# Optimization experiments

Hardware: AMD Instinct MI355X
Metric: run time of the kernel (lower is better)

Reference implementation:

```python
import jax, jax.numpy as jnp
import numpy as np

D = 1024            # BIGNET_DIM
GS = 16             # group_size
NG = D * D // GS    # groups per layer = 65536
N_LAYERS = 18       # 6 blocks * 3 linears
LORA_LAYERS = {0: 0, 6: 1, 12: 2}  # linear index -> lora slot (first linear of blocks 0,2,4)
RANK = 32
BATCH = 16384
EPS = 1e-5


def setup_inputs() -> dict:
    key = jax.random.key(0)
    ks = jax.random.split(key, 6)
    x = jax.random.normal(ks[0], (BATCH, D), dtype=jnp.float32)
    w_q = jax.random.randint(ks[1], (N_LAYERS, NG, GS), 0, 16, dtype=jnp.int32)
    w_norm = jax.random.uniform(ks[2], (N_LAYERS, NG, 1), dtype=jnp.float32)
    bias = jax.random.normal(ks[3], (N_LAYERS, D), dtype=jnp.float32) * 0.02
    lora_a = jax.random.normal(ks[4], (3, RANK, D), dtype=jnp.float32) * (1.0 / np.sqrt(D))
    lora_b = jax.random.normal(ks[5], (3, D, RANK), dtype=jnp.float32) * 0.02
    ln_w = jnp.ones((6, D), dtype=jnp.float32)
    ln_b = jnp.zeros((6, D), dtype=jnp.float32)
    return {"x": x, "w_q": w_q, "w_norm": w_norm, "bias": bias,
            "lora_a": lora_a, "lora_b": lora_b, "ln_w": ln_w, "ln_b": ln_b}


def _dequant(q, n):
    # block_dequantize_4bit: codes in [0,15] -> [-norm, +norm] per group
    return ((q.astype(jnp.float32) / 15.0) * 2.0 - 1.0) * n  # [NG, GS]


def reference(x, w_q, w_norm, bias, lora_a, lora_b, ln_w, ln_b):
    h = x
    for blk in range(6):
        for pos in range(3):
            l = blk * 3 + pos
            W = _dequant(w_q[l], w_norm[l]).reshape(D, D)  # [out, in]
            out = h @ W.T + bias[l]
            if l in LORA_LAYERS:
                i = LORA_LAYERS[l]
                out = out + (h @ lora_a[i].T) @ lora_b[i].T
            if pos < 2:
                out = jax.nn.relu(out)
            h = out
        mu = jnp.mean(h, axis=-1, keepdims=True)
        var = jnp.mean(jnp.square(h - mu), axis=-1, keepdims=True)
        h = (h - mu) * jax.lax.rsqrt(var + EPS) * ln_w[blk] + ln_b[blk]
    return h
```

## Files before the change

### kernel.cpp

```cpp
#include <hip/hip_runtime.h>
#include <cstdint>
#include <cstddef>


typedef short  bf16x8 __attribute__((ext_vector_type(8)));
typedef float  f32x4  __attribute__((ext_vector_type(4)));

__device__ __forceinline__ unsigned short f2bf(float f) {
  unsigned int u = __builtin_bit_cast(unsigned int, f);
  u += 0x7FFFu + ((u >> 16) & 1u);
  return (unsigned short)(u >> 16);
}

__device__ __forceinline__ void async_copy16(void* lds, const void* g) {
  __builtin_amdgcn_global_load_lds(
      (const __attribute__((address_space(1))) void*)(uintptr_t)(g),
      (__attribute__((address_space(3))) void*)(unsigned int)(uintptr_t)(lds),
      16, 0, 0);
}

__global__ __launch_bounds__(256) void dequant_kernel(
    const int* __restrict__ wq, const float* __restrict__ wn,
    const float* __restrict__ lora_a, const float* __restrict__ lora_b,
    unsigned short* __restrict__ Wbf) {
  const int l   = blockIdx.y;
  const int t   = threadIdx.x;
  const int blk = blockIdx.x;
  const long base = (long)l * 1048576;
  const float s = 2.0f / 15.0f;

  int4  q[4];
  float nrm[4];
#pragma unroll
  for (int k = 0; k < 4; ++k) {
    const int i4 = blk * 1024 + k * 256 + t;
    q[k]   = *(const int4*)(wq + base + (long)i4 * 4);
    nrm[k] = wn[l * 65536 + (i4 >> 2)];
  }

  float v[4][4];
#pragma unroll
  for (int k = 0; k < 4; ++k) {
    v[k][0] = ((float)q[k].x * s - 1.0f) * nrm[k];
    v[k][1] = ((float)q[k].y * s - 1.0f) * nrm[k];
    v[k][2] = ((float)q[k].z * s - 1.0f) * nrm[k];
    v[k][3] = ((float)q[k].w * s - 1.0f) * nrm[k];
  }

  const int slot = (l == 0) ? 0 : (l == 6) ? 1 : (l == 12) ? 2 : -1;
  if (slot >= 0) {
    const float* A = lora_a + slot * 32768 + t * 4;
    const float* B = lora_b + slot * 32768 + blk * 128;
#pragma unroll 8
    for (int r = 0; r < 32; ++r) {
      const float4 a4 = *(const float4*)(A + r * 1024);
#pragma unroll
      for (int k = 0; k < 4; ++k) {
        const float br = B[k * 32 + r];
        v[k][0] = fmaf(br, a4.x, v[k][0]);
        v[k][1] = fmaf(br, a4.y, v[k][1]);
        v[k][2] = fmaf(br, a4.z, v[k][2]);
        v[k][3] = fmaf(br, a4.w, v[k][3]);
      }
    }
  }

#pragma unroll
  for (int k = 0; k < 4; ++k) {
    unsigned short u[4] = {f2bf(v[k][0]), f2bf(v[k][1]),
                           f2bf(v[k][2]), f2bf(v[k][3])};
    const long e0 = base + ((long)blk * 1024 + k * 256 + t) * 4;
    *(uint2*)(Wbf + e0) = *(uint2*)u;
  }
}

__global__ __launch_bounds__(256) void cvt_bf16_kernel(
    const float* __restrict__ in, unsigned short* __restrict__ out) {
  const long b0 = (long)blockIdx.x * 4096 + threadIdx.x * 4;
  float4 v[4];
#pragma unroll
  for (int k = 0; k < 4; ++k) v[k] = *(const float4*)(in + b0 + k * 1024);
#pragma unroll
  for (int k = 0; k < 4; ++k) {
    unsigned short u[4] = {f2bf(v[k].x), f2bf(v[k].y), f2bf(v[k].z), f2bf(v[k].w)};
    *(ushort4*)(out + b0 + k * 1024) = *(ushort4*)u;
  }
}

template <int MODE>
__global__ __launch_bounds__(256, 4) void gemm_kernel(
    const unsigned short* __restrict__ H,
    const unsigned short* __restrict__ W,
    const float* __restrict__ bias,
    unsigned short* __restrict__ outb,
    float* __restrict__ outf) {
  constexpr int K = 1024;
  constexpr int NN = 1024;

  __shared__ uint4 ldsq[2048];
  char* base = (char*)ldsq;

  const int tid = threadIdx.x;
  const int w   = tid >> 6;
  const int ln  = tid & 63;
  const int b   = blockIdx.x;
  const int m0  = ((b & 7) * 16 + (b >> 6)) * 128;
  const int n0  = ((b >> 3) & 7) * 128;

  const int gc = (ln & 7) ^ (ln >> 3);
  const unsigned short* gA = H + (size_t)(m0 + w * 32 + (ln >> 3)) * K + gc * 8;
  const unsigned short* gB = W + (size_t)(n0 + w * 32 + (ln >> 3)) * K + gc * 8;
  char* ldsA = base + w * 4096;
  char* ldsB = base + 16384 + w * 4096;

  const int quad = ln >> 4;
  const int lrow = ln & 15;
  const int sw   = lrow & 7;
  const int c0   = ((quad)     ^ sw) * 16;
  const int c1   = ((quad + 4) ^ sw) * 16;
  const int wm   = (w >> 1) * 64;
  const int wn   = (w & 1) * 64;
  const char* fragA = base + (wm + lrow) * 128;
  const char* fragB = base + 16384 + (wn + lrow) * 128;

  f32x4 acc[4][4];
#pragma unroll
  for (int i = 0; i < 4; ++i)
#pragma unroll
    for (int j = 0; j < 4; ++j) acc[i][j] = (f32x4){0.f, 0.f, 0.f, 0.f};

  for (int kt = 0; kt < 16; ++kt) {
    const unsigned short* pA = gA + kt * 64;
    const unsigned short* pB = gB + kt * 64;
#pragma unroll
    for (int i = 0; i < 4; ++i) {
      async_copy16(ldsA + i * 1024, pA + (size_t)i * 8 * K);
      async_copy16(ldsB + i * 1024, pB + (size_t)i * 8 * K);
    }
    __syncthreads();
#pragma unroll
    for (int kk = 0; kk < 2; ++kk) {
      const int co = kk ? c1 : c0;
      bf16x8 af[4], bg[4];
#pragma unroll
      for (int mt = 0; mt < 4; ++mt)
        af[mt] = *(const bf16x8*)(fragA + mt * 2048 + co);
#pragma unroll
      for (int nt = 0; nt < 4; ++nt)
        bg[nt] = *(const bf16x8*)(fragB + nt * 2048 + co);
#pragma unroll
      for (int mt = 0; mt < 4; ++mt)
#pragma unroll
        for (int nt = 0; nt < 4; ++nt)
          acc[mt][nt] = __builtin_amdgcn_mfma_f32_16x16x32_bf16(
              af[mt], bg[nt], acc[mt][nt], 0, 0, 0);
    }
    __syncthreads();
  }

#pragma unroll
  for (int nt = 0; nt < 4; ++nt) {
    const int n = n0 + wn + nt * 16 + lrow;
    const float bs = bias[n];
#pragma unroll
    for (int mt = 0; mt < 4; ++mt) {
      const int mb = m0 + wm + mt * 16 + quad * 4;
      f32x4 v = acc[mt][nt];
#pragma unroll
      for (int r = 0; r < 4; ++r) {
        float o = v[r] + bs;
        if (MODE == 0) o = fmaxf(o, 0.0f);
        if (MODE == 1) {
          outf[(size_t)(mb + r) * NN + n] = o;
        } else {
          outb[(size_t)(mb + r) * NN + n] = f2bf(o);
        }
      }
    }
  }
}

__global__ __launch_bounds__(256) void ln_kernel(
    const float* __restrict__ in, const float* __restrict__ lnw,
    const float* __restrict__ lnb, unsigned short* __restrict__ outb,
    float* __restrict__ outf, int wbf, int wf32) {
  const int wv = threadIdx.x >> 6;
  const int ln = threadIdx.x & 63;
  const int row = blockIdx.x * 4 + wv;
  const float* p = in + (size_t)row * 1024;

  float4 v[4];
  float s = 0.f, q = 0.f;
#pragma unroll
  for (int c = 0; c < 4; ++c) {
    v[c] = *(const float4*)(p + c * 256 + ln * 4);
    s += v[c].x + v[c].y + v[c].z + v[c].w;
    q += v[c].x * v[c].x + v[c].y * v[c].y + v[c].z * v[c].z + v[c].w * v[c].w;
  }
#pragma unroll
  for (int off = 32; off; off >>= 1) {
    s += __shfl_xor(s, off);
    q += __shfl_xor(q, off);
  }
  const float mu  = s * (1.0f / 1024.0f);
  const float var = q * (1.0f / 1024.0f) - mu * mu;
  const float rs  = rsqrtf(var + 1e-5f);

#pragma unroll
  for (int c = 0; c < 4; ++c) {
    const int col = c * 256 + ln * 4;
    const float4 w4 = *(const float4*)(lnw + col);
    const float4 b4 = *(const float4*)(lnb + col);
    const float y0 = (v[c].x - mu) * rs * w4.x + b4.x;
    const float y1 = (v[c].y - mu) * rs * w4.y + b4.y;
    const float y2 = (v[c].z - mu) * rs * w4.z + b4.z;
    const float y3 = (v[c].w - mu) * rs * w4.w + b4.w;
    if (wbf) {
      unsigned short u[4] = {f2bf(y0), f2bf(y1), f2bf(y2), f2bf(y3)};
      *(ushort4*)(outb + (size_t)row * 1024 + col) = *(ushort4*)u;
    }
    if (wf32) {
      float4 y = make_float4(y0, y1, y2, y3);
      *(float4*)(outf + (size_t)row * 1024 + col) = y;
    }
  }
}

__global__ __launch_bounds__(256) void ln_bf16_kernel(
    const unsigned short* __restrict__ in, const float* __restrict__ lnw,
    const float* __restrict__ lnb, unsigned short* __restrict__ outb) {
  const int wv = threadIdx.x >> 6;
  const int ln = threadIdx.x & 63;
  const int row = blockIdx.x * 4 + wv;
  const unsigned short* p = in + (size_t)row * 1024 + ln * 16;

  const uint4 r0 = *(const uint4*)(p);
  const uint4 r1 = *(const uint4*)(p + 8);
  const unsigned ru[8] = {r0.x, r0.y, r0.z, r0.w, r1.x, r1.y, r1.z, r1.w};

  float f[16];
#pragma unroll
  for (int i = 0; i < 8; ++i) {
    f[2 * i]     = __builtin_bit_cast(float, ru[i] << 16);
    f[2 * i + 1] = __builtin_bit_cast(float, ru[i] & 0xffff0000u);
  }

  float s = 0.f, q = 0.f;
#pragma unroll
  for (int i = 0; i < 16; ++i) { s += f[i]; q += f[i] * f[i]; }
#pragma unroll
  for (int off = 32; off; off >>= 1) {
    s += __shfl_xor(s, off);
    q += __shfl_xor(q, off);
  }
  const float mu  = s * (1.0f / 1024.0f);
  const float var = q * (1.0f / 1024.0f) - mu * mu;
  const float rs  = rsqrtf(var + 1e-5f);

  const float* wp = lnw + ln * 16;
  const float* bp = lnb + ln * 16;
  unsigned o[8];
#pragma unroll
  for (int i = 0; i < 8; ++i) {
    const float y0 = (f[2 * i]     - mu) * rs * wp[2 * i]     + bp[2 * i];
    const float y1 = (f[2 * i + 1] - mu) * rs * wp[2 * i + 1] + bp[2 * i + 1];
    o[i] = (unsigned)f2bf(y0) | ((unsigned)f2bf(y1) << 16);
  }
  unsigned short* dst = outb + (size_t)row * 1024 + ln * 16;
  *(uint4*)(dst)     = make_uint4(o[0], o[1], o[2], o[3]);
  *(uint4*)(dst + 8) = make_uint4(o[4], o[5], o[6], o[7]);
}

extern "C" void kernel_launch(void* const* d_in, const int* in_sizes, int n_in,
                              void* d_out, int out_size, void* d_ws, size_t ws_size,
                              hipStream_t stream) {
  const float* x    = (const float*)d_in[0];
  const int*   wq   = (const int*)d_in[1];
  const float* wn   = (const float*)d_in[2];
  const float* bias = (const float*)d_in[3];
  const float* la   = (const float*)d_in[4];
  const float* lb   = (const float*)d_in[5];
  const float* lnw  = (const float*)d_in[6];
  const float* lnb  = (const float*)d_in[7];
  float* out = (float*)d_out;

  char* ws = (char*)d_ws;
  unsigned short* Wbf = (unsigned short*)ws;
  unsigned short* hA  = (unsigned short*)(ws + 37748736);
  unsigned short* hB  = (unsigned short*)(ws + 37748736 + 33554432);

  dequant_kernel<<<dim3(256, 18), 256, 0, stream>>>(wq, wn, la, lb, Wbf);
  cvt_bf16_kernel<<<4096, 256, 0, stream>>>(x, hA);

  for (int blk = 0; blk < 6; ++blk) {
    const int l = blk * 3;
    gemm_kernel<0><<<1024, 256, 0, stream>>>(
        hA, Wbf + (size_t)l * 1048576, bias + l * 1024, hB, nullptr);
    gemm_kernel<0><<<1024, 256, 0, stream>>>(
        hB, Wbf + (size_t)(l + 1) * 1048576, bias + (l + 1) * 1024, hA, nullptr);
    if (blk < 5) {
      gemm_kernel<2><<<1024, 256, 0, stream>>>(
          hA, Wbf + (size_t)(l + 2) * 1048576, bias + (l + 2) * 1024, hB, nullptr);
      ln_bf16_kernel<<<4096, 256, 0, stream>>>(
          hB, lnw + blk * 1024, lnb + blk * 1024, hA);
    } else {
      gemm_kernel<1><<<1024, 256, 0, stream>>>(
          hA, Wbf + (size_t)(l + 2) * 1048576, bias + (l + 2) * 1024, nullptr, out);
      ln_kernel<<<4096, 256, 0, stream>>>(
          out, lnw + blk * 1024, lnb + blk * 1024, nullptr, out, 0, 1);
    }
  }
}
```

Before: 922.5 us.

## Swap MFMA operands for vectorized epilogue stores and precompute LoRA product

Adds a SWAP variant of the GEMM that exchanges the MFMA A/B operands. Each lane then holds four consecutive output columns, so the epilogue can write bias-added results as packed vector stores instead of scattered scalar stores. The variant is used only for even blocks, which looks like an A/B experiment. The LoRA B·A product is moved out of the dequant kernel into a separate kernel that writes a dense fp32 matrix into the hB scratch buffer, and dequant then simply adds it. This adds an extra kernel launch and roughly 12 MB of traffic in exchange for removing redundant FMA loops in the dequant kernel.

```diff
diff --git a/kernel.cpp b/kernel.cpp
--- a/kernel.cpp
+++ b/kernel.cpp
@@ -19,9 +19,44 @@
       16, 0, 0);
 }
 
+__global__ __launch_bounds__(256) void lora_kernel(
+    const float* __restrict__ lora_a,
+    const float* __restrict__ lora_b,
+    float* __restrict__ LA) {
+  const int slot = blockIdx.y;
+  const int o0   = blockIdx.x * 4;
+  const int t    = threadIdx.x;
+  const float* A = lora_a + slot * 32768 + t * 4;
+  const float* B = lora_b + slot * 32768 + o0 * 32;
+
+  float acc[4][4];
+#pragma unroll
+  for (int k = 0; k < 4; ++k)
+#pragma unroll
+    for (int j = 0; j < 4; ++j) acc[k][j] = 0.f;
+
+#pragma unroll 8
+  for (int r = 0; r < 32; ++r) {
+    const float4 a4 = *(const float4*)(A + r * 1024);
+#pragma unroll
+    for (int k = 0; k < 4; ++k) {
+      const float br = B[k * 32 + r];
+      acc[k][0] = fmaf(br, a4.x, acc[k][0]);
+      acc[k][1] = fmaf(br, a4.y, acc[k][1]);
+      acc[k][2] = fmaf(br, a4.z, acc[k][2]);
+      acc[k][3] = fmaf(br, a4.w, acc[k][3]);
+    }
+  }
+#pragma unroll
+  for (int k = 0; k < 4; ++k) {
+    float4 o = make_float4(acc[k][0], acc[k][1], acc[k][2], acc[k][3]);
+    *(float4*)(LA + (size_t)slot * 1048576 + (size_t)(o0 + k) * 1024 + t * 4) = o;
+  }
+}
+
 __global__ __launch_bounds__(256) void dequant_kernel(
     const int* __restrict__ wq, const float* __restrict__ wn,
-    const float* __restrict__ lora_a, const float* __restrict__ lora_b,
+    const float* __restrict__ LA,
     unsigned short* __restrict__ Wbf) {
   const int l   = blockIdx.y;
   const int t   = threadIdx.x;
@@ -29,13 +64,24 @@
   const long base = (long)l * 1048576;
   const float s = 2.0f / 15.0f;
 
+  const int slot = (l == 0) ? 0 : (l == 6) ? 1 : (l == 12) ? 2 : -1;
+
   int4  q[4];
   float nrm[4];
+  float4 c4[4];
 #pragma unroll
   for (int k = 0; k < 4; ++k) {
     const int i4 = blk * 1024 + k * 256 + t;
     q[k]   = *(const int4*)(wq + base + (long)i4 * 4);
     nrm[k] = wn[l * 65536 + (i4 >> 2)];
+  }
+  if (slot >= 0) {
+    const float* LAp = LA + (size_t)slot * 1048576;
+#pragma unroll
+    for (int k = 0; k < 4; ++k) {
+      const int i4 = blk * 1024 + k * 256 + t;
+      c4[k] = *(const float4*)(LAp + (size_t)i4 * 4);
+    }
   }
 
   float v[4][4];
@@ -46,22 +92,11 @@
     v[k][2] = ((float)q[k].z * s - 1.0f) * nrm[k];
     v[k][3] = ((float)q[k].w * s - 1.0f) * nrm[k];
   }
-
-  const int slot = (l == 0) ? 0 : (l == 6) ? 1 : (l == 12) ? 2 : -1;
   if (slot >= 0) {
-    const float* A = lora_a + slot * 32768 + t * 4;
-    const float* B = lora_b + slot * 32768 + blk * 128;
-#pragma unroll 8
-    for (int r = 0; r < 32; ++r) {
-      const float4 a4 = *(const float4*)(A + r * 1024);
-#pragma unroll
-      for (int k = 0; k < 4; ++k) {
-        const float br = B[k * 32 + r];
-        v[k][0] = fmaf(br, a4.x, v[k][0]);
-        v[k][1] = fmaf(br, a4.y, v[k][1]);
-        v[k][2] = fmaf(br, a4.z, v[k][2]);
-        v[k][3] = fmaf(br, a4.w, v[k][3]);
-      }
+#pragma unroll
+    for (int k = 0; k < 4; ++k) {
+      v[k][0] += c4[k].x; v[k][1] += c4[k].y;
+      v[k][2] += c4[k].z; v[k][3] += c4[k].w;
     }
   }
 
@@ -87,7 +122,7 @@
   }
 }
 
-template <int MODE>
+template <int MODE, int SWAP>
 __global__ __launch_bounds__(256, 4) void gemm_kernel(
     const unsigned short* __restrict__ H,
     const unsigned short* __restrict__ W,
@@ -151,29 +186,60 @@
 #pragma unroll
       for (int mt = 0; mt < 4; ++mt)
 #pragma unroll
-        for (int nt = 0; nt < 4; ++nt)
-          acc[mt][nt] = __builtin_amdgcn_mfma_f32_16x16x32_bf16(
-              af[mt], bg[nt], acc[mt][nt], 0, 0, 0);
+        for (int nt = 0; nt < 4; ++nt) {
+          if (SWAP) {
+            acc[mt][nt] = __builtin_amdgcn_mfma_f32_16x16x32_bf16(
+                bg[nt], af[mt], acc[mt][nt], 0, 0, 0);
+          } else {
+            acc[mt][nt] = __builtin_amdgcn_mfma_f32_16x16x32_bf16(
+                af[mt], bg[nt], acc[mt][nt], 0, 0, 0);
+          }
+        }
     }
     __syncthreads();
   }
 
-#pragma unroll
-  for (int nt = 0; nt < 4; ++nt) {
-    const int n = n0 + wn + nt * 16 + lrow;
-    const float bs = bias[n];
+  if (SWAP) {
 #pragma unroll
     for (int mt = 0; mt < 4; ++mt) {
-      const int mb = m0 + wm + mt * 16 + quad * 4;
-      f32x4 v = acc[mt][nt];
-#pragma unroll
-      for (int r = 0; r < 4; ++r) {
-        float o = v[r] + bs;
-        if (MODE == 0) o = fmaxf(o, 0.0f);
+      const size_t row = (size_t)(m0 + wm + mt * 16 + lrow);
+#pragma unroll
+      for (int nt = 0; nt < 4; ++nt) {
+        const int nb = n0 + wn + nt * 16 + quad * 4;
+        const float4 bs = *(const float4*)(bias + nb);
+        const f32x4 v = acc[mt][nt];
+        float o0 = v[0] + bs.x, o1 = v[1] + bs.y;
+        float o2 = v[2] + bs.z, o3 = v[3] + bs.w;
+        if (MODE == 0) {
+          o0 = fmaxf(o0, 0.0f); o1 = fmaxf(o1, 0.0f);
+          o2 = fmaxf(o2, 0.0f); o3 = fmaxf(o3, 0.0f);
+        }
         if (MODE == 1) {
-          outf[(size_t)(mb + r) * NN + n] = o;
+          *(float4*)(outf + row * NN + nb) = make_float4(o0, o1, o2, o3);
         } else {
-          outb[(size_t)(mb + r) * NN + n] = f2bf(o);
+          unsigned short u[4] = {f2bf(o0), f2bf(o1), f2bf(o2), f2bf(o3)};
+          *(uint2*)(outb + row * NN + nb) = *(uint2*)u;
+        }
+      }
+    }
+  } else {
+#pragma unroll
+    for (int nt = 0; nt < 4; ++nt) {
+      const int n = n0 + wn + nt * 16 + lrow;
+      const float bs = bias[n];
+#pragma unroll
+      for (int mt = 0; mt < 4; ++mt) {
+        const int mb = m0 + wm + mt * 16 + quad * 4;
+        f32x4 v = acc[mt][nt];
+#pragma unroll
+        for (int r = 0; r < 4; ++r) {
+          float o = v[r] + bs;
+          if (MODE == 0) o = fmaxf(o, 0.0f);
+          if (MODE == 1) {
+            outf[(size_t)(mb + r) * NN + n] = o;
+          } else {
+            outb[(size_t)(mb + r) * NN + n] = f2bf(o);
+          }
         }
       }
     }
@@ -288,23 +354,38 @@
   unsigned short* Wbf = (unsigned short*)ws;
   unsigned short* hA  = (unsigned short*)(ws + 37748736);
   unsigned short* hB  = (unsigned short*)(ws + 37748736 + 33554432);
-
-  dequant_kernel<<<dim3(256, 18), 256, 0, stream>>>(wq, wn, la, lb, Wbf);
+  float* LA = (float*)hB;
+
+  lora_kernel<<<dim3(256, 3), 256, 0, stream>>>(la, lb, LA);
+  dequant_kernel<<<dim3(256, 18), 256, 0, stream>>>(wq, wn, LA, Wbf);
   cvt_bf16_kernel<<<4096, 256, 0, stream>>>(x, hA);
 
   for (int blk = 0; blk < 6; ++blk) {
     const int l = blk * 3;
-    gemm_kernel<0><<<1024, 256, 0, stream>>>(
-        hA, Wbf + (size_t)l * 1048576, bias + l * 1024, hB, nullptr);
-    gemm_kernel<0><<<1024, 256, 0, stream>>>(
-        hB, Wbf + (size_t)(l + 1) * 1048576, bias + (l + 1) * 1024, hA, nullptr);
-    if (blk < 5) {
-      gemm_kernel<2><<<1024, 256, 0, stream>>>(
+    if ((blk & 1) == 0) {
+      gemm_kernel<0, 1><<<1024, 256, 0, stream>>>(
+          hA, Wbf + (size_t)l * 1048576, bias + l * 1024, hB, nullptr);
+      gemm_kernel<0, 1><<<1024, 256, 0, stream>>>(
+          hB, Wbf + (size_t)(l + 1) * 1048576, bias + (l + 1) * 1024, hA, nullptr);
+      gemm_kernel<2, 1><<<1024, 256, 0, stream>>>(
+          hA, Wbf + (size_t)(l + 2) * 1048576, bias + (l + 2) * 1024, hB, nullptr);
+      ln_bf16_kernel<<<4096, 256, 0, stream>>>(
+          hB, lnw + blk * 1024, lnb + blk * 1024, hA);
+    } else if (blk < 5) {
+      gemm_kernel<0, 0><<<1024, 256, 0, stream>>>(
+          hA, Wbf + (size_t)l * 1048576, bias + l * 1024, hB, nullptr);
+      gemm_kernel<0, 0><<<1024, 256, 0, stream>>>(
+          hB, Wbf + (size_t)(l + 1) * 1048576, bias + (l + 1) * 1024, hA, nullptr);
+      gemm_kernel<2, 0><<<1024, 256, 0, stream>>>(
           hA, Wbf + (size_t)(l + 2) * 1048576, bias + (l + 2) * 1024, hB, nullptr);
       ln_bf16_kernel<<<4096, 256, 0, stream>>>(
           hB, lnw + blk * 1024, lnb + blk * 1024, hA);
     } else {
-      gemm_kernel<1><<<1024, 256, 0, stream>>>(
+      gemm_kernel<0, 0><<<1024, 256, 0, stream>>>(
+          hA, Wbf + (size_t)l * 1048576, bias + l * 1024, hB, nullptr);
+      gemm_kernel<0, 0><<<1024, 256, 0, stream>>>(
+          hB, Wbf + (size_t)(l + 1) * 1048576, bias + (l + 1) * 1024, hA, nullptr);
+      gemm_kernel<1, 0><<<1024, 256, 0, stream>>>(
           hA, Wbf + (size_t)(l + 2) * 1048576, bias + (l + 2) * 1024, nullptr, out);
       ln_kernel<<<4096, 256, 0, stream>>>(
           out, lnw + blk * 1024, lnb + blk * 1024, nullptr, out, 0, 1);
```

After: 978.2 us. 6.0% more time.
